# Kernel optimization log

Hardware: AMD Instinct MI355X
Metric: run time of the kernel (lower is better)

## Reference

```python
import jax, jax.numpy as jnp
import numpy as np

B, C, H, W = 4, 512, 96, 96
NH = 8
HD = C // NH
NC = 128
D = 768
L = H * W
EPS = 1e-5  # torch LayerNorm default


def _l2n(x, axis):
    # F.normalize: x / max(||x||, 1e-12)
    return x / jnp.maximum(jnp.linalg.norm(x, axis=axis, keepdims=True), 1e-12)


def _ln2d(x, g, b):
    # LayerNorm2d: normalize over channel dim of (B,C,H,W)
    mu = x.mean(1, keepdims=True)
    var = ((x - mu) ** 2).mean(1, keepdims=True)
    return (x - mu) / jnp.sqrt(var + EPS) * g[None, :, None, None] + b[None, :, None, None]


def _conv1x1(x, w):
    return jnp.einsum('oc,bchw->bohw', w, x)


def setup_inputs() -> dict:
    key = jax.random.key(0)
    ks = jax.random.split(key, 9)
    s = 0.02
    return {
        'img_feats': jax.random.normal(ks[0], (B, C, H, W), jnp.float32),
        'cls_embs': jax.random.normal(ks[1], (NC, D), jnp.float32),
        'cls_logits': jax.random.normal(ks[2], (B, NC), jnp.float32),
        'seg_logits': jax.random.normal(ks[3], (B, 1, H, W), jnp.float32),
        'gamma_g': jnp.ones((D,), jnp.float32), 'beta_g': jnp.zeros((D,), jnp.float32),
        'gamma_f': jnp.ones((C,), jnp.float32), 'beta_f': jnp.zeros((C,), jnp.float32),
        'attn_scale': jnp.ones((NH, 1, 1), jnp.float32),
        'Wg': jax.random.normal(ks[4], (C, D), jnp.float32) * s,
        'Wqkv': jax.random.normal(ks[5], (3 * C, C), jnp.float32) * s,
        'Wo': jax.random.normal(ks[6], (C, C), jnp.float32) * s,
        'bo': jnp.zeros((C,), jnp.float32),
        'gamma_n': jnp.ones((C,), jnp.float32), 'beta_n': jnp.zeros((C,), jnp.float32),
        'W1': jax.random.normal(ks[7], (C, C), jnp.float32) * s, 'b1': jnp.zeros((C,), jnp.float32),
        'W2': jax.random.normal(ks[8], (C, C), jnp.float32) * s, 'b2': jnp.zeros((C,), jnp.float32),
    }


def reference(img_feats, cls_embs, cls_logits, seg_logits, gamma_g, beta_g,
              gamma_f, beta_f, attn_scale, Wg, Wqkv, Wo, bo, gamma_n, beta_n,
              W1, b1, W2, b2):
    xn = _ln2d(img_feats, gamma_f, beta_f)
    # guide LayerNorm over embedding dim
    mu = cls_embs.mean(-1, keepdims=True)
    var = ((cls_embs - mu) ** 2).mean(-1, keepdims=True)
    cn = (cls_embs - mu) / jnp.sqrt(var + EPS) * gamma_g + beta_g
    g = (cn @ Wg.T).reshape(NC, NH, HD)  # nc nh hd

    qkv = _conv1x1(xn, Wqkv).reshape(B, 3, NH, HD, L)
    q, k, v = qkv[:, 0], qkv[:, 1], qkv[:, 2]  # each (B,NH,HD,L)

    # cosine guide map + min-max normalization + softmax-weighted aggregation over classes
    gm = jnp.einsum('nhd,bhdl->bhnl', _l2n(g, -1), _l2n(q, -2))
    gm = gm - gm.min(-1, keepdims=True)
    gm = gm / gm.max(-1, keepdims=True)
    gm = (jax.nn.softmax(gm, axis=2) * gm).sum(2, keepdims=True)  # (B,NH,1,L)

    # auxiliary guide map from cls logits + masked pooling of k
    cls_obj = jnp.einsum('nhd,bn->bhd', g, cls_logits)
    mask = jax.nn.sigmoid(seg_logits)  # (B,1,H,W)
    seg_obj = (mask * k.reshape(B, C, H, W)).sum((2, 3)) / mask.sum((2, 3))  # (B,C)
    obj = _l2n(cls_obj + seg_obj.reshape(B, NH, HD), -1)
    aux = jnp.einsum('bhd,bhdl->bhl', obj, _l2n(k, -2))[:, :, None, :]
    aux = aux - aux.min(-1, keepdims=True)
    aux = aux / aux.max(-1, keepdims=True)
    gm = gm * aux

    v = gm * v
    # channel (transposed) cosine attention: (B,NH,HD,HD)
    attn = jnp.einsum('bhdl,bhel->bhde', _l2n(q, -1), _l2n(k, -1)) * attn_scale
    out = jnp.einsum('bhde,bhel->bhdl', jax.nn.softmax(attn, -1), v).reshape(B, C, H, W)

    x = img_feats + _conv1x1(out, Wo) + bo[None, :, None, None]
    # ConvMlp with pre-norm: LayerNorm2d -> 1x1 conv -> GELU -> 1x1 conv
    fin = _ln2d(x, gamma_n, beta_n)
    h = jax.nn.gelu(_conv1x1(fin, W1) + b1[None, :, None, None], approximate=False)
    return x + _conv1x1(h, W2) + b2[None, :, None, None]
```

## Files before the change

### kernel.cpp

```cpp
#include <hip/hip_runtime.h>
#include <hip/hip_bf16.h>
#include <math.h>

#define BB 4
#define CC 512
#define NHEAD 8
#define HDIM 64
#define NCLS 128
#define DD 768
#define LL 9216
#define BLPIX 36864
#define EPSV 1e-5f
#define GMBLK 144
#define AUXBLK 36
#define LSPLIT 8

typedef __hip_bfloat16 bf16;
typedef __attribute__((ext_vector_type(8))) short short8v;
typedef __attribute__((ext_vector_type(4))) short short4v;
typedef __attribute__((ext_vector_type(4))) float f32x4;

__device__ __forceinline__ float bf2f(bf16 v){ return __bfloat162float(v); }
__device__ __forceinline__ bf16 f2bf(float v){ return __float2bfloat16(v); }
__device__ __forceinline__ short bfbits(float v){ bf16 b = __float2bfloat16(v); return *reinterpret_cast<short*>(&b); }

__global__ void ln_stats_k(const float* __restrict__ X, float* __restrict__ mu, float* __restrict__ rs){
  int idx = blockIdx.x * blockDim.x + threadIdx.x;
  if (idx >= BLPIX) return;
  int b = idx / LL, l = idx % LL;
  const float* p = X + (size_t)b * CC * LL + l;
  float s = 0.f, ss = 0.f;
  #pragma unroll 8
  for (int c = 0; c < CC; c++){ float v = p[(size_t)c * LL]; s += v; ss += v * v; }
  float m = s * (1.0f / CC);
  float var = ss * (1.0f / CC) - m * m;
  mu[idx] = m; rs[idx] = rsqrtf(var + EPSV);
}

__global__ __launch_bounds__(256) void lnT_k(const float* __restrict__ X,
    const float* __restrict__ mu, const float* __restrict__ rs,
    const float* __restrict__ lng, const float* __restrict__ lnb,
    bf16* __restrict__ out){
  __shared__ float t[64][65];
  int c0 = blockIdx.x * 64;
  int p0 = blockIdx.y * 64;
  int b = p0 / LL;
  int l0 = p0 - b * LL;
  int tid = threadIdx.x;
  #pragma unroll
  for (int i = 0; i < 16; i++){
    int idx = i * 256 + tid;
    int cl = idx >> 6, ll2 = idx & 63;
    t[cl][ll2] = X[(size_t)b * CC * LL + (size_t)(c0 + cl) * LL + l0 + ll2];
  }
  __syncthreads();
  int pr = tid >> 4;
  int cc = (tid & 15) * 4;
  #pragma unroll
  for (int i = 0; i < 4; i++){
    int pl = pr + i * 16;
    int p = p0 + pl;
    float m = mu[p], r = rs[p];
    short4v pk;
    #pragma unroll
    for (int e = 0; e < 4; e++){
      int c = c0 + cc + e;
      float v = (t[cc + e][pl] - m) * r * lng[c] + lnb[c];
      pk[e] = bfbits(v);
    }
    *(short4v*)&out[(size_t)p * CC + c0 + cc] = pk;
  }
}

__global__ void wcast_k(const float* __restrict__ wqkv, const float* __restrict__ wo,
                        const float* __restrict__ w1, const float* __restrict__ w2,
                        bf16* __restrict__ oq, bf16* __restrict__ oo,
                        bf16* __restrict__ o1, bf16* __restrict__ o2){
  int i = blockIdx.x * 256 + threadIdx.x;
  int e = i * 4;
  const float* src; bf16* dst; int off;
  if (e < 786432){ src = wqkv; dst = oq; off = e; }
  else if (e < 1048576){ src = wo; dst = oo; off = e - 786432; }
  else if (e < 1310720){ src = w1; dst = o1; off = e - 1048576; }
  else { src = w2; dst = o2; off = e - 1310720; }
  float4 v = *reinterpret_cast<const float4*>(src + off);
  short4v pk;
  pk[0] = bfbits(v.x); pk[1] = bfbits(v.y); pk[2] = bfbits(v.z); pk[3] = bfbits(v.w);
  *(short4v*)&dst[off] = pk;
}

template<int MODE>
__global__ __launch_bounds__(256, 2) void mgemm_k(
    const bf16* __restrict__ A,
    const bf16* __restrict__ B,
    const float* __restrict__ resid,
    const float* __restrict__ bias,
    bf16* __restrict__ qo, bf16* __restrict__ ko, bf16* __restrict__ vo,
    float* __restrict__ xo,
    bf16* __restrict__ ho)
{
  __shared__ short Asm[128 * 64];
  __shared__ short Bsm[128 * 64];
  int tid = threadIdx.x;
  int lane = tid & 63, wv = tid >> 6;
  int wr = wv >> 1, wc = wv & 1;
  int r15 = lane & 15, g = lane >> 4, h7 = lane & 7;
  int m0 = blockIdx.x * 128, n0 = blockIdx.y * 128;
  int srow = tid >> 3, skkg = tid & 7;
  int sslot = ((skkg ^ (srow & 7))) * 8;

  f32x4 acc[4][4];
  #pragma unroll
  for (int i = 0; i < 4; i++)
    #pragma unroll
    for (int j = 0; j < 4; j++) acc[i][j] = (f32x4){0.f, 0.f, 0.f, 0.f};

  short8v pa[4], pb[4];
  auto loadAB = [&](int it){
    int k0 = it * 64;
    #pragma unroll
    for (int r = 0; r < 4; r++){
      pa[r] = *reinterpret_cast<const short8v*>(A + (size_t)(m0 + r * 32 + srow) * 512 + k0 + skkg * 8);
      pb[r] = *reinterpret_cast<const short8v*>(B + (size_t)(n0 + r * 32 + srow) * 512 + k0 + skkg * 8);
    }
  };

  loadAB(0);
  for (int it = 0; it < 8; ++it){
    __syncthreads();
    #pragma unroll
    for (int r = 0; r < 4; r++){
      int row = r * 32 + srow;
      *(short8v*)&Asm[row * 64 + sslot] = pa[r];
      *(short8v*)&Bsm[row * 64 + sslot] = pb[r];
    }
    __syncthreads();
    if (it < 7) loadAB(it + 1);
    #pragma unroll
    for (int s = 0; s < 2; s++){
      int slot = ((s * 4 + g) ^ h7) * 8;
      short8v af[4], bf_[4];
      #pragma unroll
      for (int i = 0; i < 4; i++){
        af[i]  = *(const short8v*)&Asm[(wr * 64 + i * 16 + r15) * 64 + slot];
        bf_[i] = *(const short8v*)&Bsm[(wc * 64 + i * 16 + r15) * 64 + slot];
      }
      #pragma unroll
      for (int i = 0; i < 4; i++)
        #pragma unroll
        for (int j = 0; j < 4; j++){
          if (MODE == 2)
            acc[i][j] = __builtin_amdgcn_mfma_f32_16x16x32_bf16(bf_[i], af[j], acc[i][j], 0, 0, 0);
          else
            acc[i][j] = __builtin_amdgcn_mfma_f32_16x16x32_bf16(af[i], bf_[j], acc[i][j], 0, 0, 0);
        }
    }
  }

  int bIdx = n0 / LL;
  int lbase = n0 - bIdx * LL;
  if (MODE == 0){
    int part = m0 >> 9;
    if (part < 2){
      bf16* dst = (part == 0) ? qo : ko;
      int chb = (m0 & 511) + wr * 64;
      #pragma unroll
      for (int i = 0; i < 4; i++)
        #pragma unroll
        for (int j = 0; j < 4; j++){
          int l = lbase + wc * 64 + j * 16 + r15;
          #pragma unroll
          for (int e = 0; e < 4; e++){
            int ch = chb + i * 16 + g * 4 + e;
            dst[(size_t)bIdx * CC * LL + (size_t)ch * LL + l] = f2bf(acc[i][j][e]);
          }
        }
    } else {
      int chb = (m0 & 511) + wr * 64;
      #pragma unroll
      for (int i = 0; i < 4; i++)
        #pragma unroll
        for (int j = 0; j < 4; j++){
          int l = lbase + wc * 64 + j * 16 + r15;
          int ch = chb + i * 16 + g * 4;
          short4v pk;
          #pragma unroll
          for (int e = 0; e < 4; e++) pk[e] = bfbits(acc[i][j][e]);
          *(short4v*)&vo[((size_t)bIdx * LL + l) * CC + ch] = pk;
        }
    }
  } else if (MODE == 1 || MODE == 3){
    #pragma unroll
    for (int i = 0; i < 4; i++)
      #pragma unroll
      for (int j = 0; j < 4; j++){
        int l = lbase + wc * 64 + j * 16 + r15;
        #pragma unroll
        for (int e = 0; e < 4; e++){
          int m = m0 + wr * 64 + i * 16 + g * 4 + e;
          size_t o = (size_t)bIdx * CC * LL + (size_t)m * LL + l;
          xo[o] = resid[o] + acc[i][j][e] + bias[m];
        }
      }
  } else {
    #pragma unroll
    for (int i = 0; i < 4; i++)
      #pragma unroll
      for (int j = 0; j < 4; j++){
        int mm = m0 + wr * 64 + j * 16 + r15;
        float bv = bias[mm];
        #pragma unroll
        for (int e = 0; e < 4; e++){
          int n = n0 + wc * 64 + i * 16 + g * 4 + e;
          float t = acc[i][j][e] + bv;
          float gv = 0.5f * t * (1.0f + erff(t * 0.70710678118654752f));
          ho[(size_t)n * CC + mm] = f2bf(gv);
        }
      }
  }
}

__global__ void rownorm_k(const bf16* __restrict__ q, const bf16* __restrict__ k,
                          float* __restrict__ qn, float* __restrict__ kn){
  __shared__ float red[256];
  int row = blockIdx.x;
  const bf16* src = (row < 2048) ? q : k;
  int r = (row < 2048) ? row : row - 2048;
  const bf16* p = src + (size_t)r * LL;
  float s = 0.f;
  for (int i = threadIdx.x; i < LL; i += 256){ float v = bf2f(p[i]); s += v * v; }
  red[threadIdx.x] = s; __syncthreads();
  for (int st = 128; st > 0; st >>= 1){ if (threadIdx.x < st) red[threadIdx.x] += red[threadIdx.x + st]; __syncthreads(); }
  if (threadIdx.x == 0){
    float nv = fmaxf(sqrtf(red[0]), 1e-12f);
    if (row < 2048) qn[r] = nv; else kn[r] = nv;
  }
}

__global__ void clsg_k(const float* __restrict__ cls_embs, const float* __restrict__ gamma_g,
                       const float* __restrict__ beta_g, const float* __restrict__ Wg,
                       float* __restrict__ g, bf16* __restrict__ gnb){
  __shared__ float cn[DD];
  __shared__ float red[256];
  __shared__ float gsh[CC];
  __shared__ float nrm[NHEAD];
  int n = blockIdx.x;
  const float* e = cls_embs + (size_t)n * DD;
  float s = 0.f, ss = 0.f;
  for (int i = threadIdx.x; i < DD; i += 256){ float v = e[i]; s += v; ss += v * v; }
  red[threadIdx.x] = s; __syncthreads();
  for (int st = 128; st > 0; st >>= 1){ if (threadIdx.x < st) red[threadIdx.x] += red[threadIdx.x + st]; __syncthreads(); }
  float mean = red[0] / DD; __syncthreads();
  red[threadIdx.x] = ss; __syncthreads();
  for (int st = 128; st > 0; st >>= 1){ if (threadIdx.x < st) red[threadIdx.x] += red[threadIdx.x + st]; __syncthreads(); }
  float var = red[0] / DD - mean * mean;
  float rstd = rsqrtf(var + EPSV);
  __syncthreads();
  for (int i = threadIdx.x; i < DD; i += 256) cn[i] = (e[i] - mean) * rstd * gamma_g[i] + beta_g[i];
  __syncthreads();
  for (int c = threadIdx.x; c < CC; c += 256){
    const float* w = Wg + (size_t)c * DD;
    float a = 0.f;
    #pragma unroll 8
    for (int d = 0; d < DD; d++) a += cn[d] * w[d];
    gsh[c] = a;
  }
  __syncthreads();
  if (threadIdx.x < NHEAD){
    float a = 0.f;
    for (int d = 0; d < HDIM; d++){ float v = gsh[threadIdx.x * HDIM + d]; a += v * v; }
    nrm[threadIdx.x] = fmaxf(sqrtf(a), 1e-12f);
  }
  __syncthreads();
  for (int c = threadIdx.x; c < CC; c += 256){
    g[(size_t)n * CC + c] = gsh[c];
    gnb[(size_t)n * CC + c] = f2bf(gsh[c] / nrm[c >> 6]);
  }
}

__global__ void clsobj_k(const float* __restrict__ g, const float* __restrict__ cls_l,
                         float* __restrict__ cls_obj){
  int idx = blockIdx.x * 256 + threadIdx.x;
  if (idx >= BB * CC) return;
  int b = idx >> 9, c = idx & 511;
  float a = 0.f;
  for (int n = 0; n < NCLS; n++) a += g[(size_t)n * CC + c] * cls_l[b * NCLS + n];
  cls_obj[idx] = a;
}

__global__ __launch_bounds__(256) void gm1_k(const bf16* __restrict__ q, const bf16* __restrict__ gnb,
        float* __restrict__ pmin, float* __restrict__ pmax){
  __shared__ bf16 qs[64 * 68];
  __shared__ float sspart[4][64];
  __shared__ float rq[64];
  int bh = blockIdx.x, lt = blockIdx.y;
  int l0 = lt * 64;
  int t = threadIdx.x;
  int b = bh >> 3, h = bh & 7;
  int w = t >> 6, lane = t & 63, r15 = lane & 15, g = lane >> 4;
  const bf16* qp = q + (size_t)b * CC * LL + (size_t)h * HDIM * LL + l0;
  #pragma unroll
  for (int i2 = 0; i2 < 4; i2++){
    int idx = t + i2 * 256;
    int d = idx >> 4, lch = (idx & 15) * 4;
    short4v vv = *reinterpret_cast<const short4v*>(qp + (size_t)d * LL + lch);
    *(short4v*)&qs[d * 68 + lch] = vv;
  }
  __syncthreads();
  {
    int l = t & 63, dg = t >> 6;
    float ss = 0.f;
    #pragma unroll
    for (int dd = 0; dd < 16; dd++){ float v = bf2f(qs[(dg * 16 + dd) * 68 + l]); ss += v * v; }
    sspart[dg][l] = ss;
  }
  __syncthreads();
  if (t < 64){
    float ss = sspart[0][t] + sspart[1][t] + sspart[2][t] + sspart[3][t];
    rq[t] = 1.0f / fmaxf(sqrtf(ss), 1e-12f);
  }
  __syncthreads();
  short8v ag[2][2];
  #pragma unroll
  for (int i = 0; i < 2; i++)
    #pragma unroll
    for (int kt = 0; kt < 2; kt++)
      ag[i][kt] = *reinterpret_cast<const short8v*>(gnb + (size_t)(w * 32 + i * 16 + r15) * CC + h * 64 + kt * 32 + g * 8);
  short8v bq[4][2];
  #pragma unroll
  for (int j = 0; j < 4; j++){
    float rqv = rq[j * 16 + r15];
    #pragma unroll
    for (int kt = 0; kt < 2; kt++){
      short8v bb;
      #pragma unroll
      for (int jj = 0; jj < 8; jj++){
        int d = kt * 32 + g * 8 + jj;
        bb[jj] = bfbits(bf2f(qs[d * 68 + j * 16 + r15]) * rqv);
      }
      bq[j][kt] = bb;
    }
  }
  f32x4 acc[2][4];
  #pragma unroll
  for (int i = 0; i < 2; i++)
    #pragma unroll
    for (int j = 0; j < 4; j++) acc[i][j] = (f32x4){0.f,0.f,0.f,0.f};
  #pragma unroll
  for (int kt = 0; kt < 2; kt++)
    #pragma unroll
    for (int i = 0; i < 2; i++)
      #pragma unroll
      for (int j = 0; j < 4; j++)
        acc[i][j] = __builtin_amdgcn_mfma_f32_16x16x32_bf16(ag[i][kt], bq[j][kt], acc[i][j], 0, 0, 0);
  #pragma unroll
  for (int i = 0; i < 2; i++)
    #pragma unroll
    for (int e = 0; e < 4; e++){
      float mn = acc[i][0][e], mx = acc[i][0][e];
      #pragma unroll
      for (int j = 1; j < 4; j++){ mn = fminf(mn, acc[i][j][e]); mx = fmaxf(mx, acc[i][j][e]); }
      #pragma unroll
      for (int msk = 1; msk < 16; msk <<= 1){
        mn = fminf(mn, __shfl_xor(mn, msk));
        mx = fmaxf(mx, __shfl_xor(mx, msk));
      }
      if (r15 == 0){
        int n = w * 32 + i * 16 + g * 4 + e;
        pmin[((size_t)bh * 128 + n) * GMBLK + lt] = mn;
        pmax[((size_t)bh * 128 + n) * GMBLK + lt] = mx;
      }
    }
}

__global__ void gmred_k(const float* __restrict__ pmin, const float* __restrict__ pmax,
                        float* __restrict__ gmin, float* __restrict__ gms){
  __shared__ float rmn[64], rmx[64];
  int row = blockIdx.x;
  float mn = 1e30f, mx = -1e30f;
  for (int i = threadIdx.x; i < GMBLK; i += 64){
    mn = fminf(mn, pmin[(size_t)row * GMBLK + i]);
    mx = fmaxf(mx, pmax[(size_t)row * GMBLK + i]);
  }
  rmn[threadIdx.x] = mn; rmx[threadIdx.x] = mx; __syncthreads();
  for (int st = 32; st > 0; st >>= 1){
    if (threadIdx.x < st){
      rmn[threadIdx.x] = fminf(rmn[threadIdx.x], rmn[threadIdx.x + st]);
      rmx[threadIdx.x] = fmaxf(rmx[threadIdx.x], rmx[threadIdx.x + st]);
    }
    __syncthreads();
  }
  if (threadIdx.x == 0){ gmin[row] = rmn[0]; gms[row] = rmx[0] - rmn[0]; }
}

__global__ void seg_k(const float* __restrict__ seg, const bf16* __restrict__ k, float* __restrict__ seg_num){
  __shared__ float red[256];
  int bc = blockIdx.x;
  int b = bc >> 9;
  const bf16* p = k + (size_t)bc * LL;
  const float* sp = seg + (size_t)b * LL;
  float s = 0.f;
  for (int i = threadIdx.x; i < LL; i += 256){
    float m = 1.0f / (1.0f + expf(-sp[i]));
    s += m * bf2f(p[i]);
  }
  red[threadIdx.x] = s; __syncthreads();
  for (int st = 128; st > 0; st >>= 1){ if (threadIdx.x < st) red[threadIdx.x] += red[threadIdx.x + st]; __syncthreads(); }
  if (threadIdx.x == 0) seg_num[bc] = red[0];
}

__global__ void segden_k(const float* __restrict__ seg, float* __restrict__ den){
  __shared__ float red[256];
  int b = blockIdx.x;
  const float* sp = seg + (size_t)b * LL;
  float s = 0.f;
  for (int i = threadIdx.x; i < LL; i += 256) s += 1.0f / (1.0f + expf(-sp[i]));
  red[threadIdx.x] = s; __syncthreads();
  for (int st = 128; st > 0; st >>= 1){ if (threadIdx.x < st) red[threadIdx.x] += red[threadIdx.x + st]; __syncthreads(); }
  if (threadIdx.x == 0) den[b] = red[0];
}

__global__ void obj_k(const float* __restrict__ cls_obj, const float* __restrict__ seg_num,
                      const float* __restrict__ den, float* __restrict__ obj){
  __shared__ float sval[2048];
  __shared__ float nrm[32];
  int tid = threadIdx.x;
  #pragma unroll
  for (int i = 0; i < 8; i++){
    int idx = tid + i * 256;
    int b = idx >> 9;
    sval[idx] = cls_obj[idx] + seg_num[idx] / den[b];
  }
  __syncthreads();
  if (tid < 32){
    float s = 0.f;
    for (int d = 0; d < 64; d++){ float v = sval[tid * 64 + d]; s += v * v; }
    nrm[tid] = fmaxf(sqrtf(s), 1e-12f);
  }
  __syncthreads();
  #pragma unroll
  for (int i = 0; i < 8; i++){
    int idx = tid + i * 256;
    obj[idx] = sval[idx] / nrm[idx >> 6];
  }
}

__global__ void aux_k(const bf16* __restrict__ k, const float* __restrict__ obj, float* __restrict__ aux,
                      float* __restrict__ pmin, float* __restrict__ pmax){
  __shared__ float os[64];
  __shared__ float rmn[256], rmx[256];
  int bh = blockIdx.x, lt = blockIdx.y;
  int b = bh >> 3, h = bh & 7;
  int l = lt * 256 + threadIdx.x;
  if (threadIdx.x < 64) os[threadIdx.x] = obj[bh * 64 + threadIdx.x];
  __syncthreads();
  const bf16* kp = k + (size_t)b * CC * LL + (size_t)h * HDIM * LL + l;
  float ss = 0.f, dot = 0.f;
  #pragma unroll 8
  for (int d = 0; d < 64; d++){ float v = bf2f(kp[(size_t)d * LL]); ss += v * v; dot += os[d] * v; }
  float av = dot / fmaxf(sqrtf(ss), 1e-12f);
  aux[(size_t)bh * LL + l] = av;
  rmn[threadIdx.x] = av; rmx[threadIdx.x] = av; __syncthreads();
  for (int st = 128; st > 0; st >>= 1){
    if (threadIdx.x < st){
      rmn[threadIdx.x] = fminf(rmn[threadIdx.x], rmn[threadIdx.x + st]);
      rmx[threadIdx.x] = fmaxf(rmx[threadIdx.x], rmx[threadIdx.x + st]);
    }
    __syncthreads();
  }
  if (threadIdx.x == 0){ pmin[bh * AUXBLK + lt] = rmn[0]; pmax[bh * AUXBLK + lt] = rmx[0]; }
}

__global__ void auxred_k(const float* __restrict__ pmin, const float* __restrict__ pmax,
                         float* __restrict__ amin, float* __restrict__ ams){
  __shared__ float rmn[64], rmx[64];
  int bh = blockIdx.x;
  float mn = 1e30f, mx = -1e30f;
  for (int i = threadIdx.x; i < AUXBLK; i += 64){
    mn = fminf(mn, pmin[bh * AUXBLK + i]);
    mx = fmaxf(mx, pmax[bh * AUXBLK + i]);
  }
  rmn[threadIdx.x] = mn; rmx[threadIdx.x] = mx; __syncthreads();
  for (int st = 32; st > 0; st >>= 1){
    if (threadIdx.x < st){
      rmn[threadIdx.x] = fminf(rmn[threadIdx.x], rmn[threadIdx.x + st]);
      rmx[threadIdx.x] = fmaxf(rmx[threadIdx.x], rmx[threadIdx.x + st]);
    }
    __syncthreads();
  }
  if (threadIdx.x == 0){ amin[bh] = rmn[0]; ams[bh] = rmx[0] - rmn[0]; }
}

__global__ __launch_bounds__(256) void attn_k(const bf16* __restrict__ q, const bf16* __restrict__ k,
                                              float* __restrict__ part){
  __shared__ float red[4 * 4096];
  int ls = blockIdx.x, bh = blockIdx.y;
  int b = bh >> 3, h = bh & 7;
  int t = threadIdx.x;
  int w = t >> 6, lane = t & 63, r15 = lane & 15, g = lane >> 4;
  const bf16* qp = q + (size_t)b * CC * LL + (size_t)h * HDIM * LL;
  const bf16* kp = k + (size_t)b * CC * LL + (size_t)h * HDIM * LL;
  int kbase = ls * 1152 + w * 288;
  f32x4 acc[4][4];
  #pragma unroll
  for (int i = 0; i < 4; i++)
    #pragma unroll
    for (int j = 0; j < 4; j++) acc[i][j] = (f32x4){0.f,0.f,0.f,0.f};
  for (int ks = 0; ks < 9; ks++){
    int koff = kbase + ks * 32 + g * 8;
    short8v aq[4], bk[4];
    #pragma unroll
    for (int i = 0; i < 4; i++) aq[i] = *reinterpret_cast<const short8v*>(qp + (size_t)(i * 16 + r15) * LL + koff);
    #pragma unroll
    for (int j = 0; j < 4; j++) bk[j] = *reinterpret_cast<const short8v*>(kp + (size_t)(j * 16 + r15) * LL + koff);
    #pragma unroll
    for (int i = 0; i < 4; i++)
      #pragma unroll
      for (int j = 0; j < 4; j++)
        acc[i][j] = __builtin_amdgcn_mfma_f32_16x16x32_bf16(aq[i], bk[j], acc[i][j], 0, 0, 0);
  }
  #pragma unroll
  for (int i = 0; i < 4; i++)
    #pragma unroll
    for (int j = 0; j < 4; j++)
      #pragma unroll
      for (int e = 0; e < 4; e++)
        red[w * 4096 + (i * 16 + g * 4 + e) * 64 + j * 16 + r15] = acc[i][j][e];
  __syncthreads();
  #pragma unroll
  for (int it = 0; it < 16; it++){
    int idx = t + it * 256;
    part[((size_t)(bh * LSPLIT + ls)) * 4096 + idx] = red[idx] + red[4096 + idx] + red[8192 + idx] + red[12288 + idx];
  }
}

__global__ void smax_k(const float* __restrict__ part, const float* __restrict__ qn,
                       const float* __restrict__ kn, const float* __restrict__ scale,
                       bf16* __restrict__ Pb){
  __shared__ float As[64 * 65];
  int bh = blockIdx.x;
  int h = bh & 7;
  int tid = threadIdx.x;
  #pragma unroll
  for (int i = 0; i < 16; i++){
    int cell = tid + i * 256;
    int d = cell >> 6, e = cell & 63;
    float s = 0.f;
    #pragma unroll
    for (int ls = 0; ls < LSPLIT; ls++) s += part[((size_t)(bh * LSPLIT + ls)) * 4096 + cell];
    As[d * 65 + e] = s * scale[h] / (qn[bh * 64 + d] * kn[bh * 64 + e]);
  }
  __syncthreads();
  if (tid < 64){
    int d = tid;
    float mx = -1e30f;
    for (int e = 0; e < 64; e++) mx = fmaxf(mx, As[d * 65 + e]);
    float sum = 0.f;
    for (int e = 0; e < 64; e++){ float ev = expf(As[d * 65 + e] - mx); As[d * 65 + e] = ev; sum += ev; }
    float inv = 1.0f / sum;
    for (int e = 0; e < 64; e++) Pb[(size_t)bh * 4096 + d * 64 + e] = f2bf(As[d * 65 + e] * inv);
  }
}

__global__ __launch_bounds__(256) void pv_k(const bf16* __restrict__ q, const bf16* __restrict__ gnb,
      const float* __restrict__ aux,
      const float* __restrict__ gmin, const float* __restrict__ gms,
      const float* __restrict__ amin, const float* __restrict__ ams,
      const bf16* __restrict__ Pb, const bf16* __restrict__ vT, bf16* __restrict__ outT){
  __shared__ bf16 qs[64 * 68];
  __shared__ float sspart[4][64];
  __shared__ float rq[64];
  __shared__ float gminS[128], rgmsS[128];
  __shared__ float separt[4][64], setpart[4][64];
  __shared__ float wl[64];
  int bh = blockIdx.x, lt = blockIdx.y;
  int l0 = lt * 64;
  int t = threadIdx.x;
  int b = bh >> 3, h = bh & 7;
  int w = t >> 6, lane = t & 63, r15 = lane & 15, g = lane >> 4;
  if (t < 128){ gminS[t] = gmin[bh * 128 + t]; rgmsS[t] = 1.0f / gms[bh * 128 + t]; }
  const bf16* qp = q + (size_t)b * CC * LL + (size_t)h * HDIM * LL + l0;
  #pragma unroll
  for (int i2 = 0; i2 < 4; i2++){
    int idx = t + i2 * 256;
    int d = idx >> 4, lch = (idx & 15) * 4;
    short4v vv = *reinterpret_cast<const short4v*>(qp + (size_t)d * LL + lch);
    *(short4v*)&qs[d * 68 + lch] = vv;
  }
  __syncthreads();
  {
    int l = t & 63, dg = t >> 6;
    float ss = 0.f;
    #pragma unroll
    for (int dd = 0; dd < 16; dd++){ float v = bf2f(qs[(dg * 16 + dd) * 68 + l]); ss += v * v; }
    sspart[dg][l] = ss;
  }
  __syncthreads();
  if (t < 64){
    float ss = sspart[0][t] + sspart[1][t] + sspart[2][t] + sspart[3][t];
    rq[t] = 1.0f / fmaxf(sqrtf(ss), 1e-12f);
  }
  __syncthreads();
  short8v ag[2][2];
  #pragma unroll
  for (int i = 0; i < 2; i++)
    #pragma unroll
    for (int kt = 0; kt < 2; kt++)
      ag[i][kt] = *reinterpret_cast<const short8v*>(gnb + (size_t)(w * 32 + i * 16 + r15) * CC + h * 64 + kt * 32 + g * 8);
  short8v bq[4][2];
  #pragma unroll
  for (int j = 0; j < 4; j++){
    float rqv = rq[j * 16 + r15];
    #pragma unroll
    for (int kt = 0; kt < 2; kt++){
      short8v bb;
      #pragma unroll
      for (int jj = 0; jj < 8; jj++){
        int d = kt * 32 + g * 8 + jj;
        bb[jj] = bfbits(bf2f(qs[d * 68 + j * 16 + r15]) * rqv);
      }
      bq[j][kt] = bb;
    }
  }
  f32x4 acc[2][4];
  #pragma unroll
  for (int i = 0; i < 2; i++)
    #pragma unroll
    for (int j = 0; j < 4; j++) acc[i][j] = (f32x4){0.f,0.f,0.f,0.f};
  #pragma unroll
  for (int kt = 0; kt < 2; kt++)
    #pragma unroll
    for (int i = 0; i < 2; i++)
      #pragma unroll
      for (int j = 0; j < 4; j++)
        acc[i][j] = __builtin_amdgcn_mfma_f32_16x16x32_bf16(ag[i][kt], bq[j][kt], acc[i][j], 0, 0, 0);
  float seL[4] = {0.f,0.f,0.f,0.f}, setL[4] = {0.f,0.f,0.f,0.f};
  #pragma unroll
  for (int i = 0; i < 2; i++)
    #pragma unroll
    for (int j = 0; j < 4; j++)
      #pragma unroll
      for (int e = 0; e < 4; e++){
        int n = w * 32 + i * 16 + g * 4 + e;
        float tt = (acc[i][j][e] - gminS[n]) * rgmsS[n];
        float ee = __expf(tt);
        seL[j] += ee; setL[j] += ee * tt;
      }
  #pragma unroll
  for (int j = 0; j < 4; j++){
    seL[j] += __shfl_xor(seL[j], 16); seL[j] += __shfl_xor(seL[j], 32);
    setL[j] += __shfl_xor(setL[j], 16); setL[j] += __shfl_xor(setL[j], 32);
  }
  if (g == 0){
    #pragma unroll
    for (int j = 0; j < 4; j++){ separt[w][j * 16 + r15] = seL[j]; setpart[w][j * 16 + r15] = setL[j]; }
  }
  __syncthreads();
  if (t < 64){
    float se = separt[0][t] + separt[1][t] + separt[2][t] + separt[3][t];
    float st = setpart[0][t] + setpart[1][t] + setpart[2][t] + setpart[3][t];
    float gmred = st / se;
    float auxn = (aux[(size_t)bh * LL + l0 + t] - amin[bh]) / ams[bh];
    wl[t] = gmred * auxn;
  }
  __syncthreads();
  short8v ap[4][2];
  #pragma unroll
  for (int i = 0; i < 4; i++)
    #pragma unroll
    for (int kt = 0; kt < 2; kt++)
      ap[i][kt] = *reinterpret_cast<const short8v*>(Pb + (size_t)bh * 4096 + (i * 16 + r15) * 64 + kt * 32 + g * 8);
  const bf16* vrow = vT + ((size_t)b * LL + l0 + w * 16 + r15) * CC + h * 64;
  short8v bv[2];
  #pragma unroll
  for (int kt = 0; kt < 2; kt++) bv[kt] = *reinterpret_cast<const short8v*>(vrow + kt * 32 + g * 8);
  f32x4 oacc[4];
  #pragma unroll
  for (int i = 0; i < 4; i++) oacc[i] = (f32x4){0.f,0.f,0.f,0.f};
  #pragma unroll
  for (int kt = 0; kt < 2; kt++)
    #pragma unroll
    for (int i = 0; i < 4; i++)
      oacc[i] = __builtin_amdgcn_mfma_f32_16x16x32_bf16(ap[i][kt], bv[kt], oacc[i], 0, 0, 0);
  float wlv = wl[w * 16 + r15];
  bf16* orow = outT + ((size_t)b * LL + l0 + w * 16 + r15) * CC + h * 64;
  #pragma unroll
  for (int i = 0; i < 4; i++){
    short4v pk;
    #pragma unroll
    for (int e = 0; e < 4; e++) pk[e] = bfbits(oacc[i][e] * wlv);
    *(short4v*)&orow[i * 16 + g * 4] = pk;
  }
}

extern "C" void kernel_launch(void* const* d_in, const int* in_sizes, int n_in,
                              void* d_out, int out_size, void* d_ws, size_t ws_size,
                              hipStream_t stream){
  const float* img        = (const float*)d_in[0];
  const float* cls_embs   = (const float*)d_in[1];
  const float* cls_logits = (const float*)d_in[2];
  const float* seg        = (const float*)d_in[3];
  const float* gamma_g    = (const float*)d_in[4];
  const float* beta_g     = (const float*)d_in[5];
  const float* gamma_f    = (const float*)d_in[6];
  const float* beta_f     = (const float*)d_in[7];
  const float* attn_scale = (const float*)d_in[8];
  const float* Wg         = (const float*)d_in[9];
  const float* Wqkv       = (const float*)d_in[10];
  const float* Wo         = (const float*)d_in[11];
  const float* bo         = (const float*)d_in[12];
  const float* gamma_n    = (const float*)d_in[13];
  const float* beta_n     = (const float*)d_in[14];
  const float* W1         = (const float*)d_in[15];
  const float* b1         = (const float*)d_in[16];
  const float* W2         = (const float*)d_in[17];
  const float* b2         = (const float*)d_in[18];
  float* outp = (float*)d_out;
  (void)in_sizes; (void)n_in; (void)out_size;

  char* wsb = (char*)d_ws;
  size_t off = 0;
  auto alloc = [&](size_t bytes)->char*{
    char* p = wsb + off;
    off += (bytes + 255) & ~(size_t)255;
    return p;
  };
  float* mu1   = (float*)alloc((size_t)BLPIX * 4);
  float* rs1   = (float*)alloc((size_t)BLPIX * 4);
  float* qn    = (float*)alloc(2048 * 4);
  float* kn    = (float*)alloc(2048 * 4);
  float* gbuf  = (float*)alloc((size_t)NCLS * CC * 4);
  bf16*  gnbb  = (bf16*)alloc((size_t)NCLS * CC * 2);
  float* clsov = (float*)alloc(2048 * 4);
  float* segn  = (float*)alloc(2048 * 4);
  float* segd  = (float*)alloc(256);
  float* objv  = (float*)alloc(2048 * 4);
  float* gminp = (float*)alloc((size_t)32 * 128 * GMBLK * 4);
  float* gmaxp = (float*)alloc((size_t)32 * 128 * GMBLK * 4);
  float* gminv = (float*)alloc(4096 * 4);
  float* gmsv  = (float*)alloc(4096 * 4);
  float* auxv  = (float*)alloc((size_t)32 * LL * 4);
  float* apmin = (float*)alloc(32 * AUXBLK * 4);
  float* apmax = (float*)alloc(32 * AUXBLK * 4);
  float* aminv = (float*)alloc(256);
  float* amsv  = (float*)alloc(256);
  bf16*  Pb    = (bf16*)alloc((size_t)32 * 4096 * 2);
  float* apart = (float*)alloc((size_t)32 * LSPLIT * 4096 * 4);
  bf16* qb    = (bf16*)alloc((size_t)BB * CC * LL * 2);
  bf16* kb    = (bf16*)alloc((size_t)BB * CC * LL * 2);
  bf16* wqkvb = (bf16*)alloc((size_t)1536 * 512 * 2);
  bf16* wob   = (bf16*)alloc((size_t)512 * 512 * 2);
  bf16* w1b   = (bf16*)alloc((size_t)512 * 512 * 2);
  bf16* w2b   = (bf16*)alloc((size_t)512 * 512 * 2);
  bf16* vT  = (bf16*)d_out;
  bf16* xnT = (bf16*)((char*)d_out + (size_t)BB * CC * LL * 2);
  bf16* outT = kb;
  bf16* xnT2 = qb;
  bf16* hbT  = kb;
  float* xb  = outp;
  if (off > ws_size) return;

  ln_stats_k<<<BLPIX / 256, 256, 0, stream>>>(img, mu1, rs1);
  wcast_k<<<1536, 256, 0, stream>>>(Wqkv, Wo, W1, W2, wqkvb, wob, w1b, w2b);
  lnT_k<<<dim3(8, 576), 256, 0, stream>>>(img, mu1, rs1, gamma_f, beta_f, xnT);
  mgemm_k<0><<<dim3(12, 288), 256, 0, stream>>>(wqkvb, xnT, nullptr, nullptr,
      qb, kb, vT, nullptr, nullptr);
  rownorm_k<<<4096, 256, 0, stream>>>(qb, kb, qn, kn);
  clsg_k<<<NCLS, 256, 0, stream>>>(cls_embs, gamma_g, beta_g, Wg, gbuf, gnbb);
  clsobj_k<<<8, 256, 0, stream>>>(gbuf, cls_logits, clsov);
  gm1_k<<<dim3(32, GMBLK), 256, 0, stream>>>(qb, gnbb, gminp, gmaxp);
  gmred_k<<<4096, 64, 0, stream>>>(gminp, gmaxp, gminv, gmsv);
  seg_k<<<2048, 256, 0, stream>>>(seg, kb, segn);
  segden_k<<<BB, 256, 0, stream>>>(seg, segd);
  obj_k<<<1, 256, 0, stream>>>(clsov, segn, segd, objv);
  aux_k<<<dim3(32, AUXBLK), 256, 0, stream>>>(kb, objv, auxv, apmin, apmax);
  auxred_k<<<32, 64, 0, stream>>>(apmin, apmax, aminv, amsv);
  attn_k<<<dim3(LSPLIT, 32), 256, 0, stream>>>(qb, kb, apart);
  smax_k<<<32, 256, 0, stream>>>(apart, qn, kn, attn_scale, Pb);
  pv_k<<<dim3(32, GMBLK), 256, 0, stream>>>(qb, gnbb, auxv, gminv, gmsv, aminv, amsv, Pb, vT, outT);
  mgemm_k<1><<<dim3(4, 288), 256, 0, stream>>>(wob, outT, img, bo,
      nullptr, nullptr, nullptr, xb, nullptr);
  ln_stats_k<<<BLPIX / 256, 256, 0, stream>>>(xb, mu1, rs1);
  lnT_k<<<dim3(8, 576), 256, 0, stream>>>(xb, mu1, rs1, gamma_n, beta_n, xnT2);
  mgemm_k<2><<<dim3(4, 288), 256, 0, stream>>>(w1b, xnT2, nullptr, b1,
      nullptr, nullptr, nullptr, nullptr, hbT);
  mgemm_k<3><<<dim3(4, 288), 256, 0, stream>>>(w2b, hbT, xb, b2,
      nullptr, nullptr, nullptr, outp, nullptr);
}
```

Baseline: 540.5 us.

## Fuse second LayerNorm into Wo GEMM epilogue and W1 GEMM operand load

```diff
diff --git a/kernel.cpp b/kernel.cpp
--- a/kernel.cpp
+++ b/kernel.cpp
@@ -23,6 +23,7 @@
 __device__ __forceinline__ float bf2f(bf16 v){ return __bfloat162float(v); }
 __device__ __forceinline__ bf16 f2bf(float v){ return __float2bfloat16(v); }
 __device__ __forceinline__ short bfbits(float v){ bf16 b = __float2bfloat16(v); return *reinterpret_cast<short*>(&b); }
+__device__ __forceinline__ float s2f(short s){ bf16 b = *reinterpret_cast<bf16*>(&s); return __bfloat162float(b); }
 
 __global__ void ln_stats_k(const float* __restrict__ X, float* __restrict__ mu, float* __restrict__ rs){
   int idx = blockIdx.x * blockDim.x + threadIdx.x;
@@ -89,23 +90,47 @@
   *(short4v*)&dst[off] = pk;
 }
 
+__global__ void statsred_k(const float2* __restrict__ statp, float* __restrict__ mu, float* __restrict__ rs){
+  int p = blockIdx.x * 256 + threadIdx.x;
+  if (p >= BLPIX) return;
+  float s = 0.f, ss = 0.f;
+  #pragma unroll
+  for (int part = 0; part < 4; part++){
+    float2 v = statp[part * BLPIX + p];
+    s += v.x; ss += v.y;
+  }
+  float m = s * (1.0f / CC);
+  float var = ss * (1.0f / CC) - m * m;
+  mu[p] = m; rs[p] = rsqrtf(var + EPSV);
+}
+
 template<int MODE>
 __global__ __launch_bounds__(256, 2) void mgemm_k(
     const bf16* __restrict__ A,
     const bf16* __restrict__ B,
-    const float* __restrict__ resid,
+    const float* __restrict__ residf,
+    const bf16*  __restrict__ residb,
     const float* __restrict__ bias,
+    const float* __restrict__ mu, const float* __restrict__ rs,
+    const float* __restrict__ lng, const float* __restrict__ lnb,
+    float2* __restrict__ statp,
     bf16* __restrict__ qo, bf16* __restrict__ ko, bf16* __restrict__ vo,
+    bf16* __restrict__ xT_out,
     float* __restrict__ xo,
     bf16* __restrict__ ho)
 {
   __shared__ short Asm[128 * 64];
   __shared__ short Bsm[128 * 64];
+  __shared__ float sred[4][4][16][2];
   int tid = threadIdx.x;
   int lane = tid & 63, wv = tid >> 6;
   int wr = wv >> 1, wc = wv & 1;
   int r15 = lane & 15, g = lane >> 4, h7 = lane & 7;
-  int m0 = blockIdx.x * 128, n0 = blockIdx.y * 128;
+  int gx = gridDim.x;
+  int flat = blockIdx.y * gx + blockIdx.x;
+  int cpx = (gx * gridDim.y) >> 3;
+  int swz = (flat & 7) * cpx + (flat >> 3);
+  int m0 = (swz % gx) * 128, n0 = (swz / gx) * 128;
   int srow = tid >> 3, skkg = tid & 7;
   int sslot = ((skkg ^ (srow & 7))) * 8;
 
@@ -118,10 +143,33 @@
   short8v pa[4], pb[4];
   auto loadAB = [&](int it){
     int k0 = it * 64;
-    #pragma unroll
-    for (int r = 0; r < 4; r++){
-      pa[r] = *reinterpret_cast<const short8v*>(A + (size_t)(m0 + r * 32 + srow) * 512 + k0 + skkg * 8);
-      pb[r] = *reinterpret_cast<const short8v*>(B + (size_t)(n0 + r * 32 + srow) * 512 + k0 + skkg * 8);
+    if (MODE == 2){
+      int c0 = k0 + skkg * 8;
+      float ga[8], be[8];
+      *(float4*)&ga[0] = *(const float4*)&lng[c0];
+      *(float4*)&ga[4] = *(const float4*)&lng[c0 + 4];
+      *(float4*)&be[0] = *(const float4*)&lnb[c0];
+      *(float4*)&be[4] = *(const float4*)&lnb[c0 + 4];
+      #pragma unroll
+      for (int r = 0; r < 4; r++){
+        pa[r] = *reinterpret_cast<const short8v*>(A + (size_t)(m0 + r * 32 + srow) * 512 + c0);
+        int rp = n0 + r * 32 + srow;
+        float mm = mu[rp], rr = rs[rp];
+        short8v raw = *reinterpret_cast<const short8v*>(B + (size_t)rp * 512 + c0);
+        short8v ov;
+        #pragma unroll
+        for (int e = 0; e < 8; e++){
+          float v = (s2f(raw[e]) - mm) * rr * ga[e] + be[e];
+          ov[e] = bfbits(v);
+        }
+        pb[r] = ov;
+      }
+    } else {
+      #pragma unroll
+      for (int r = 0; r < 4; r++){
+        pa[r] = *reinterpret_cast<const short8v*>(A + (size_t)(m0 + r * 32 + srow) * 512 + k0 + skkg * 8);
+        pb[r] = *reinterpret_cast<const short8v*>(B + (size_t)(n0 + r * 32 + srow) * 512 + k0 + skkg * 8);
+      }
     }
   };
 
@@ -189,17 +237,55 @@
           *(short4v*)&vo[((size_t)bIdx * LL + l) * CC + ch] = pk;
         }
     }
-  } else if (MODE == 1 || MODE == 3){
+  } else if (MODE == 1){
+    float sj[4] = {0.f,0.f,0.f,0.f}, ssj[4] = {0.f,0.f,0.f,0.f};
     #pragma unroll
     for (int i = 0; i < 4; i++)
       #pragma unroll
       for (int j = 0; j < 4; j++){
         int l = lbase + wc * 64 + j * 16 + r15;
+        int chm = m0 + wr * 64 + i * 16 + g * 4;
+        short4v pk;
         #pragma unroll
         for (int e = 0; e < 4; e++){
-          int m = m0 + wr * 64 + i * 16 + g * 4 + e;
+          int m = chm + e;
           size_t o = (size_t)bIdx * CC * LL + (size_t)m * LL + l;
-          xo[o] = resid[o] + acc[i][j][e] + bias[m];
+          float xv = residf[o] + acc[i][j][e] + bias[m];
+          pk[e] = bfbits(xv);
+          sj[j] += xv; ssj[j] += xv * xv;
+        }
+        *(short4v*)&xT_out[((size_t)bIdx * LL + l) * CC + chm] = pk;
+      }
+    #pragma unroll
+    for (int j = 0; j < 4; j++){
+      sj[j] += __shfl_xor(sj[j], 16); sj[j] += __shfl_xor(sj[j], 32);
+      ssj[j] += __shfl_xor(ssj[j], 16); ssj[j] += __shfl_xor(ssj[j], 32);
+    }
+    if (g == 0){
+      #pragma unroll
+      for (int j = 0; j < 4; j++){ sred[wv][j][r15][0] = sj[j]; sred[wv][j][r15][1] = ssj[j]; }
+    }
+    __syncthreads();
+    if (tid < 128){
+      int wv2 = tid >> 6, lane2 = tid & 63, j2 = lane2 >> 4, r2 = lane2 & 15;
+      float s = sred[wv2][j2][r2][0] + sred[wv2 + 2][j2][r2][0];
+      float ss2 = sred[wv2][j2][r2][1] + sred[wv2 + 2][j2][r2][1];
+      int p = n0 + wv2 * 64 + j2 * 16 + r2;
+      statp[(m0 >> 7) * BLPIX + p] = make_float2(s, ss2);
+    }
+  } else if (MODE == 3){
+    #pragma unroll
+    for (int i = 0; i < 4; i++)
+      #pragma unroll
+      for (int j = 0; j < 4; j++){
+        int l = lbase + wc * 64 + j * 16 + r15;
+        int chm = m0 + wr * 64 + i * 16 + g * 4;
+        short4v rv = *(const short4v*)&residb[((size_t)bIdx * LL + l) * CC + chm];
+        #pragma unroll
+        for (int e = 0; e < 4; e++){
+          int m = chm + e;
+          size_t o = (size_t)bIdx * CC * LL + (size_t)m * LL + l;
+          xo[o] = s2f(rv[e]) + acc[i][j][e] + bias[m];
         }
       }
   } else {
@@ -727,6 +813,7 @@
   };
   float* mu1   = (float*)alloc((size_t)BLPIX * 4);
   float* rs1   = (float*)alloc((size_t)BLPIX * 4);
+  float2* statp= (float2*)alloc((size_t)4 * BLPIX * 8);
   float* qn    = (float*)alloc(2048 * 4);
   float* kn    = (float*)alloc(2048 * 4);
   float* gbuf  = (float*)alloc((size_t)NCLS * CC * 4);
@@ -755,16 +842,15 @@
   bf16* vT  = (bf16*)d_out;
   bf16* xnT = (bf16*)((char*)d_out + (size_t)BB * CC * LL * 2);
   bf16* outT = kb;
-  bf16* xnT2 = qb;
+  bf16* xT   = qb;
   bf16* hbT  = kb;
-  float* xb  = outp;
   if (off > ws_size) return;
 
   ln_stats_k<<<BLPIX / 256, 256, 0, stream>>>(img, mu1, rs1);
   wcast_k<<<1536, 256, 0, stream>>>(Wqkv, Wo, W1, W2, wqkvb, wob, w1b, w2b);
   lnT_k<<<dim3(8, 576), 256, 0, stream>>>(img, mu1, rs1, gamma_f, beta_f, xnT);
-  mgemm_k<0><<<dim3(12, 288), 256, 0, stream>>>(wqkvb, xnT, nullptr, nullptr,
-      qb, kb, vT, nullptr, nullptr);
+  mgemm_k<0><<<dim3(12, 288), 256, 0, stream>>>(wqkvb, xnT, nullptr, nullptr, nullptr,
+      nullptr, nullptr, nullptr, nullptr, nullptr, qb, kb, vT, nullptr, nullptr, nullptr);
   rownorm_k<<<4096, 256, 0, stream>>>(qb, kb, qn, kn);
   clsg_k<<<NCLS, 256, 0, stream>>>(cls_embs, gamma_g, beta_g, Wg, gbuf, gnbb);
   clsobj_k<<<8, 256, 0, stream>>>(gbuf, cls_logits, clsov);
@@ -778,12 +864,11 @@
   attn_k<<<dim3(LSPLIT, 32), 256, 0, stream>>>(qb, kb, apart);
   smax_k<<<32, 256, 0, stream>>>(apart, qn, kn, attn_scale, Pb);
   pv_k<<<dim3(32, GMBLK), 256, 0, stream>>>(qb, gnbb, auxv, gminv, gmsv, aminv, amsv, Pb, vT, outT);
-  mgemm_k<1><<<dim3(4, 288), 256, 0, stream>>>(wob, outT, img, bo,
-      nullptr, nullptr, nullptr, xb, nullptr);
-  ln_stats_k<<<BLPIX / 256, 256, 0, stream>>>(xb, mu1, rs1);
-  lnT_k<<<dim3(8, 576), 256, 0, stream>>>(xb, mu1, rs1, gamma_n, beta_n, xnT2);
-  mgemm_k<2><<<dim3(4, 288), 256, 0, stream>>>(w1b, xnT2, nullptr, b1,
-      nullptr, nullptr, nullptr, nullptr, hbT);
-  mgemm_k<3><<<dim3(4, 288), 256, 0, stream>>>(w2b, hbT, xb, b2,
-      nullptr, nullptr, nullptr, outp, nullptr);
-}
+  mgemm_k<1><<<dim3(4, 288), 256, 0, stream>>>(wob, outT, img, nullptr, bo,
+      nullptr, nullptr, nullptr, nullptr, statp, nullptr, nullptr, nullptr, xT, nullptr, nullptr);
+  statsred_k<<<BLPIX / 256, 256, 0, stream>>>(statp, mu1, rs1);
+  mgemm_k<2><<<dim3(4, 288), 256, 0, stream>>>(w1b, xT, nullptr, nullptr, b1,
+      mu1, rs1, gamma_n, beta_n, nullptr, nullptr, nullptr, nullptr, nullptr, nullptr, hbT);
+  mgemm_k<3><<<dim3(4, 288), 256, 0, stream>>>(w2b, hbT, nullptr, xT, b2,
+      nullptr, nullptr, nullptr, nullptr, nullptr, nullptr, nullptr, nullptr, nullptr, outp, nullptr);
+}
```

Result: faster. 497.6 us (-7.9%).
